# Optimization experiments

Hardware: AMD Instinct MI355X
Metric: run time of the kernel (lower is better)

## Reference

```python
import jax, jax.numpy as jnp
import numpy as np
from jax import lax

B, S, C, L = 256, 30, 62, 169   # batch, timesteps, channels(nodes), data_seg
OG, OH = 64, 64                 # out_gcn, out_gru
K1, K2, K3 = 64, 32, 14         # depthwise kernel sizes (169-63-31-13 = 62 = C)


def setup_inputs() -> dict:
    key = jax.random.key(0)
    ks = jax.random.split(key, 26)
    def n(k, shape, s=0.05):
        return jax.random.normal(k, shape, dtype=jnp.float32) * s
    inp = {
        "x": jax.random.normal(ks[0], (B, S, C, L), dtype=jnp.float32),
        "adj": jax.random.normal(ks[1], (C, C), dtype=jnp.float32),
        # depthwise-separable conv 1 (kernel 64)
        "dw1_w": n(ks[2], (C, 1, K1)), "dw1_b": n(ks[3], (C,)),
        "pw1_w": n(ks[4], (C, C, 1)), "pw1_b": n(ks[5], (C,)),
        # depthwise-separable conv 2 (kernel 32)
        "dw2_w": n(ks[6], (C, 1, K2)), "dw2_b": n(ks[7], (C,)),
        "pw2_w": n(ks[8], (C, C, 1)), "pw2_b": n(ks[9], (C,)),
        # depthwise-separable conv 3 (kernel 14)
        "dw3_w": n(ks[10], (C, 1, K3)), "dw3_b": n(ks[11], (C,)),
        "pw3_w": n(ks[12], (C, C, 1)), "pw3_b": n(ks[13], (C,)),
        # GraphConvolution(data_seg, out_gcn): support = x @ W; out = adj @ support + b
        "gcn_w": n(ks[14], (L, OG)), "gcn_b": n(ks[15], (OG,)),
        # GRU-style gate Linears (out_gcn+out_gru -> out_gru), torch layout (out, in)
        "Wr_w": n(ks[16], (OH, OG + OH)), "Wr_b": n(ks[17], (OH,)),
        "Wu_w": n(ks[18], (OH, OG + OH)), "Wu_b": n(ks[19], (OH,)),
        "Wc_w": n(ks[20], (OH, OG + OH)), "Wc_b": n(ks[21], (OH,)),
        # extra learned gate biases b_r/b_u/b_c (init zeros in torch)
        "b_r": jnp.zeros((OH,), jnp.float32),
        "b_u": jnp.zeros((OH,), jnp.float32),
        "b_c": jnp.zeros((OH,), jnp.float32),
    }
    return inp


def _dsconv(x, dw, dwb, pw, pwb):
    # x: (b, c, l); depthwise (groups=c, valid padding) then pointwise 1x1
    dn = ("NCH", "OIH", "NCH")
    y = lax.conv_general_dilated(x, dw, (1,), "VALID", dimension_numbers=dn,
                                 feature_group_count=x.shape[1]) + dwb[None, :, None]
    y = lax.conv_general_dilated(y, pw, (1,), "VALID", dimension_numbers=dn) + pwb[None, :, None]
    return y


def reference(x, adj, dw1_w, dw1_b, pw1_w, pw1_b, dw2_w, dw2_b, pw2_w, pw2_b,
              dw3_w, dw3_b, pw3_w, pw3_b, gcn_w, gcn_b,
              Wr_w, Wr_b, Wu_w, Wu_b, Wc_w, Wc_b, b_r, b_u, b_c):
    b, s, c, l = x.shape
    oh = b_r.shape[0]

    def step(h, xt):            # h: (b*c, oh), xt: (b, c, l)
        d = _dsconv(xt, dw1_w, dw1_b, pw1_w, pw1_b)
        d = _dsconv(d, dw2_w, dw2_b, pw2_w, pw2_b)
        d = _dsconv(d, dw3_w, dw3_b, pw3_w, pw3_b)      # (b, c, c)
        adj_t = jax.nn.sigmoid(d + adj)                  # adaptive adjacency
        support = jnp.einsum("bcl,lf->bcf", xt, gcn_w)
        g = jnp.einsum("bij,bjf->bif", adj_t, support) + gcn_b  # (b, c, og)
        gf = g.reshape(b * c, -1)
        cat = jnp.concatenate([gf, h], axis=-1)
        r = jax.nn.sigmoid(cat @ Wr_w.T + Wr_b + b_r)
        u = jax.nn.sigmoid(cat @ Wu_w.T + Wu_b + b_u)
        cc = jnp.tanh(jnp.concatenate([gf, r * h], axis=-1) @ Wc_w.T + Wc_b + b_c)
        h_new = u * h + (1.0 - u) * cc
        return h_new, None

    h0 = jnp.zeros((b * c, oh), x.dtype)
    xs = jnp.swapaxes(x, 0, 1)          # (s, b, c, l)
    h_last, _ = lax.scan(step, h0, xs)
    return h_last.reshape(b, c, oh)[:, -1, :]   # (b, out_gru)
```

## Files before the change

kernel.cpp:

```cpp
#include <hip/hip_runtime.h>
#include <math.h>

#define BB 256
#define SS 30
#define CC 62
#define LL 169
#define OG 64
#define OH 64
#define KK1 64
#define KK2 32
#define KK3 14
#define FLEN 108

typedef __attribute__((ext_vector_type(8))) short s16x8;
typedef __attribute__((ext_vector_type(4))) float f32x4;

__device__ __forceinline__ unsigned short f2bf(float f) {
    unsigned u = __float_as_uint(f);
    u += 0x7fffu + ((u >> 16) & 1u);
    return (unsigned short)(u >> 16);
}

__global__ __launch_bounds__(1024) void k_setup1(
        const float* __restrict__ dw1, const float* __restrict__ dw1b,
        const float* __restrict__ pw1, const float* __restrict__ pw1b,
        const float* __restrict__ dw2, const float* __restrict__ dw2b,
        const float* __restrict__ pw2, const float* __restrict__ pw2b,
        const float* __restrict__ dw3, const float* __restrict__ dw3b,
        const float* __restrict__ pw3, const float* __restrict__ pw3b,
        const float* __restrict__ Wr, const float* __restrict__ Wrb, const float* __restrict__ br,
        const float* __restrict__ Wu, const float* __restrict__ Wub, const float* __restrict__ bu,
        const float* __restrict__ Wc, const float* __restrict__ Wcb, const float* __restrict__ bc,
        float* __restrict__ Bmg, float* __restrict__ WtAll,
        float* __restrict__ bias192, float* __restrict__ beff) {
    __shared__ float g23[CC * KK3];
    __shared__ float Am[CC * 45];
    __shared__ float by2[CC], vals[CC];
    int tid = threadIdx.x;

    for (int idx = tid; idx < OG * 192; idx += 1024) {
        int i = idx / 192, q = idx - i * 192;
        int gate = q >> 6, f = q & 63;
        const float* W = gate == 0 ? Wr : (gate == 1 ? Wu : Wc);
        WtAll[idx] = W[f * (OG + OH) + i];
    }
    if (tid < 192) {
        int gate = tid >> 6, f = tid & 63;
        const float* Wb = gate == 0 ? Wrb : (gate == 1 ? Wub : Wcb);
        const float* bb = gate == 0 ? br  : (gate == 1 ? bu  : bc);
        bias192[tid] = Wb[f] + bb[f];
    }
    for (int idx = tid; idx < CC * KK3; idx += 1024) {
        int c1 = idx / KK3, k3 = idx - c1 * KK3;
        float s = 0.f;
        for (int c2 = 0; c2 < CC; ++c2)
            s += pw3[61 * CC + c2] * pw2[c2 * CC + c1] * dw3[c2 * KK3 + k3];
        g23[idx] = s;
    }
    if (tid < CC) {
        int c1 = tid;
        float bz1 = pw1b[c1];
        for (int c0 = 0; c0 < CC; ++c0) bz1 += pw1[c1 * CC + c0] * dw1b[c0];
        float s2 = 0.f;
        for (int k = 0; k < KK2; ++k) s2 += dw2[c1 * KK2 + k];
        by2[c1] = dw2b[c1] + bz1 * s2;
    }
    __syncthreads();
    if (tid < CC) {
        int c2 = tid;
        float bz2 = pw2b[c2];
        for (int c1 = 0; c1 < CC; ++c1) bz2 += pw2[c2 * CC + c1] * by2[c1];
        float s3 = 0.f;
        for (int k = 0; k < KK3; ++k) s3 += dw3[c2 * KK3 + k];
        vals[c2] = pw3[61 * CC + c2] * (dw3b[c2] + bz2 * s3);
    }
    for (int idx = tid; idx < CC * 45; idx += 1024) {
        int c1 = idx / 45, m = idx - c1 * 45;
        int k2lo = max(0, m - (KK3 - 1));
        int k2hi = min(KK2 - 1, m);
        float s = 0.f;
        for (int k2 = k2lo; k2 <= k2hi; ++k2)
            s += dw2[c1 * KK2 + k2] * g23[c1 * KK3 + (m - k2)];
        Am[idx] = s;
    }
    __syncthreads();
    if (tid == 0) {
        float s = pw3b[61];
        for (int c2 = 0; c2 < CC; ++c2) s += vals[c2];
        *beff = s;
    }
    for (int idx = tid; idx < CC * 45; idx += 1024) {
        int c0 = idx / 45, m = idx - c0 * 45;
        float s = 0.f;
        for (int c1 = 0; c1 < CC; ++c1) s += pw1[c1 * CC + c0] * Am[c1 * 45 + m];
        Bmg[idx] = s;
    }
}

__global__ __launch_bounds__(128) void k_setupF(
        const float* __restrict__ Bmg, const float* __restrict__ dw1,
        unsigned short* __restrict__ Ftb) {
    __shared__ float Bl[45];
    int c0 = blockIdx.x;
    int o = threadIdx.x;
    if (c0 < CC && o < 45) Bl[o] = Bmg[c0 * 45 + o];
    __syncthreads();
    if (o >= 112) return;
    float s = 0.f;
    if (c0 < CC && o < FLEN) {
        int mlo = max(0, o - (KK1 - 1));
        int mhi = min(44, o);
        for (int m = mlo; m <= mhi; ++m)
            s += Bl[m] * dw1[c0 * KK1 + (o - m)];
    }
    Ftb[o * 64 + c0] = f2bf(s);
}

#define CH_ISSUE(ch) do {                                                          \
    const int nd2 = ((ch) < 7) ? 676 : 507;                                        \
    const float* cb = xg + 1352 * (ch);                                            \
    _Pragma("unroll")                                                              \
    for (int j = 0; j < 3; ++j) {                                                  \
        int pos = tid + j * 256; if (pos > nd2 - 1) pos = nd2 - 1;                 \
        asm volatile("global_load_dwordx2 %0, %1, off"                             \
                     : "=v"(SL[(ch) & 1][j]) : "v"(cb + 2 * pos));                 \
    }                                                                              \
} while (0)

#define CH_CONSUME(ch, VM) do {                                                    \
    asm volatile("s_waitcnt vmcnt(" VM ")"                                         \
        : "+v"(SL[(ch) & 1][0]), "+v"(SL[(ch) & 1][1]), "+v"(SL[(ch) & 1][2]));    \
    {                                                                              \
        const int nd2 = ((ch) < 7) ? 676 : 507;                                    \
        uint2* cb2 = (uint2*)chunkbuf[(ch) & 1];                                   \
        _Pragma("unroll")                                                          \
        for (int j = 0; j < 3; ++j) {                                              \
            int pos = tid + j * 256; if (pos > nd2 - 1) pos = nd2 - 1;             \
            cb2[pos] = SL[(ch) & 1][j];                                            \
        }                                                                          \
    }                                                                              \
    asm volatile("s_waitcnt lgkmcnt(0)" ::: "memory");                             \
    __builtin_amdgcn_sched_barrier(0);                                             \
    __builtin_amdgcn_s_barrier();                                                  \
    {                                                                              \
        const int ncp = ((ch) < 7) ? 4 : 3;                                        \
        const unsigned* cb = (const unsigned*)chunkbuf[(ch) & 1];                  \
        int cpL = tid & 3, lb = tid >> 2;                                          \
        _Pragma("unroll")                                                          \
        for (int it = 0; it < 3; ++it) {                                           \
            int l = lb + 64 * it;                                                  \
            if (l < LL && cpL < ncp) {                                             \
                unsigned lo = cb[(2 * cpL) * LL + l];                              \
                unsigned hi = cb[(2 * cpL + 1) * LL + l];                          \
                unsigned v;                                                        \
                asm("v_cvt_pk_bf16_f32 %0, %1, %2" : "=v"(v)                       \
                    : "v"(__uint_as_float(lo)), "v"(__uint_as_float(hi)));         \
                int cp = (ch) * 4 + cpL;                                           \
                xTu[(l * 32 + cp) ^ ((l & 7) << 2)] = v;                           \
            }                                                                      \
        }                                                                          \
    }                                                                              \
    asm volatile("s_waitcnt lgkmcnt(0)" ::: "memory");                             \
    __builtin_amdgcn_sched_barrier(0);                                             \
    __builtin_amdgcn_s_barrier();                                                  \
} while (0)

__global__ __launch_bounds__(256, 3) void k_main(
        const float* __restrict__ x, const float* __restrict__ adj,
        const unsigned short* __restrict__ Ftb, const float* __restrict__ beff_p,
        const float* __restrict__ gcnw, const float* __restrict__ gcnb,
        const float* __restrict__ WtAll, const float* __restrict__ bias192,
        float* __restrict__ gates) {
    __shared__ __align__(16) unsigned short xT[176 * 64];
    __shared__ __align__(16) char chunkbuf[2][5408];
    __shared__ float dacc[4][64];
    __shared__ __align__(16) unsigned adjbf[32];
    __shared__ float wxl[176];
    __shared__ float gpart[4][64];
    __shared__ float Gl[64];
    int bt = blockIdx.x;
    int tid = threadIdx.x;
    int lane = tid & 63, wid = tid >> 6;
    int col = lane & 15, rb4 = lane >> 4;
    unsigned* xTu = (unsigned*)xT;
    const float* xg = x + (size_t)bt * (CC * LL);

    float be = *beff_p;
    float2 arow2 = make_float2(0.f, 0.f);
    if (tid < 31) arow2 = *(const float2*)(adj + 61 * CC + 2 * tid);
    const unsigned short* ap0 = Ftb + ((wid * 16 + col) * 64 + rb4 * 8);
    s16x8 pa0 = *(const s16x8*)ap0;
    s16x8 pa1 = *(const s16x8*)(ap0 + 32);
    int mt2c = wid + 4 < 7 ? wid + 4 : 6;
    const unsigned short* ap1 = Ftb + ((mt2c * 16 + col) * 64 + rb4 * 8);
    s16x8 pb0 = *(const s16x8*)(ap1);
    s16x8 pb1 = *(const s16x8*)(ap1 + 32);
    __builtin_amdgcn_sched_barrier(0);

    uint2 SL[2][3];
    CH_ISSUE(0); CH_ISSUE(1);
    for (int i = tid; i < 169; i += 256) xTu[(i * 32 + 31) ^ ((i & 7) << 2)] = 0;
    for (int i = tid; i < 224; i += 256) {
        int r = 169 + (i >> 5), dd = i & 31;
        xTu[(r * 32 + dd) ^ ((r & 7) << 2)] = 0;
    }
    ((float*)dacc)[tid] = 0.f;

    CH_CONSUME(0, "3"); CH_ISSUE(2);
    CH_CONSUME(1, "3"); CH_ISSUE(3);
    CH_CONSUME(2, "3"); CH_ISSUE(4);
    CH_CONSUME(3, "3"); CH_ISSUE(5);
    CH_CONSUME(4, "3"); CH_ISSUE(6);
    CH_CONSUME(5, "3"); CH_ISSUE(7);
    CH_CONSUME(6, "3");
    CH_CONSUME(7, "0");

    f32x4 zacc[5];
    #pragma unroll
    for (int d = 0; d < 5; ++d) zacc[d] = (f32x4){0.f, 0.f, 0.f, 0.f};
    int kb = rb4 * 16;
    int xr = (lane & 7) << 4;
    #pragma unroll
    for (int h = 0; h < 2; ++h) {
        int mt = wid + 4 * h;
        if (mt < 7) {
            s16x8 a0 = h == 0 ? pa0 : pb0;
            s16x8 a1 = h == 0 ? pa1 : pb1;
            #pragma unroll
            for (int d = 0; d < 5; ++d) {
                int nt = mt + d;
                int bbyte = ((nt * 16 + col) * 128 + kb) ^ xr;
                s16x8 b0 = *(const s16x8*)((const char*)xT + bbyte);
                s16x8 b1 = *(const s16x8*)((const char*)xT + (bbyte ^ 64));
                zacc[d] = __builtin_amdgcn_mfma_f32_16x16x32_bf16(a0, b0, zacc[d], 0, 0, 0);
                zacc[d] = __builtin_amdgcn_mfma_f32_16x16x32_bf16(a1, b1, zacc[d], 0, 0, 0);
            }
        }
    }
    int jc = col - rb4 * 4;
    #pragma unroll
    for (int d = 0; d < 5; ++d) {
        #pragma unroll
        for (int r = 0; r < 4; ++r) {
            int j = 16 * d + jc - r;
            if ((unsigned)j < 62u) atomicAdd(&dacc[rb4][j], zacc[d][r]);
        }
    }
    __syncthreads();

    if (tid < 32) {
        unsigned pk = 0;
        if (tid < 31) {
            int j0 = 2 * tid;
            float2 g0 = *(const float2*)(&dacc[0][j0]);
            float2 g1 = *(const float2*)(&dacc[1][j0]);
            float2 g2 = *(const float2*)(&dacc[2][j0]);
            float2 g3 = *(const float2*)(&dacc[3][j0]);
            float dv0 = (g0.x + g1.x) + (g2.x + g3.x) + be + arow2.x;
            float dv1 = (g0.y + g1.y) + (g2.y + g3.y) + be + arow2.y;
            float s0 = 1.f / (1.f + __expf(-dv0));
            float s1 = 1.f / (1.f + __expf(-dv1));
            asm("v_cvt_pk_bf16_f32 %0, %1, %2" : "=v"(pk) : "v"(s0), "v"(s1));
        }
        adjbf[tid] = pk;
    }
    __syncthreads();

    {
        s16x8 wa0 = *(const s16x8*)(adjbf + rb4 * 4);
        s16x8 wa1 = *(const s16x8*)(adjbf + 16 + rb4 * 4);
        #pragma unroll
        for (int q = 0; q < 3; ++q) {
            int nt = wid + 4 * q;
            if (nt < 11) {
                int bbyte = ((nt * 16 + col) * 128 + kb) ^ xr;
                s16x8 b0 = *(const s16x8*)((const char*)xT + bbyte);
                s16x8 b1 = *(const s16x8*)((const char*)xT + (bbyte ^ 64));
                f32x4 wacc = {0.f, 0.f, 0.f, 0.f};
                wacc = __builtin_amdgcn_mfma_f32_16x16x32_bf16(wa0, b0, wacc, 0, 0, 0);
                wacc = __builtin_amdgcn_mfma_f32_16x16x32_bf16(wa1, b1, wacc, 0, 0, 0);
                if (rb4 == 0) wxl[nt * 16 + col] = wacc[0];
            }
        }
    }
    __syncthreads();

    {
        int f = tid & 63, lq = tid >> 6;
        float s = 0.f;
        for (int l = lq; l < LL; l += 4) s += wxl[l] * gcnw[l * OG + f];
        gpart[lq][f] = s;
    }
    __syncthreads();
    if (tid < OG)
        Gl[tid] = gcnb[tid] + gpart[0][tid] + gpart[1][tid] + gpart[2][tid] + gpart[3][tid];
    __syncthreads();

    if (tid < 192) {
        float s = bias192[tid];
        #pragma unroll 16
        for (int k = 0; k < OG; ++k) s += Gl[k] * WtAll[k * 192 + tid];
        gates[(size_t)bt * 192 + tid] = s;
    }
}

__global__ __launch_bounds__(256) void k_scan(
        const float* __restrict__ gates,
        const float* __restrict__ Wr, const float* __restrict__ Wu, const float* __restrict__ Wc,
        float* __restrict__ out) {
    __shared__ float hl[OH], rhl[OH];
    int b = blockIdx.x;
    int tid = threadIdx.x;
    int f = tid >> 2, q = tid & 3;
    float wr[16], wu[16], wc[16];
    #pragma unroll
    for (int i = 0; i < 16; ++i) {
        int col = OG + q * 16 + i;
        wr[i] = Wr[f * (OG + OH) + col];
        wu[i] = Wu[f * (OG + OH) + col];
        wc[i] = Wc[f * (OG + OH) + col];
    }
    float h = 0.f;
    if (tid < OH) hl[tid] = 0.f;
    __syncthreads();
    for (int t = 0; t < SS; ++t) {
        const float* gp = gates + ((size_t)b * SS + t) * 192;
        float gr = gp[f];
        float gu = gp[64 + f];
        float gc = gp[128 + f];
        float rv = 0.f, uv = 0.f;
        #pragma unroll
        for (int i = 0; i < 16; ++i) {
            float hv = hl[q * 16 + i];
            rv += wr[i] * hv;
            uv += wu[i] * hv;
        }
        rv += __shfl_xor(rv, 1); rv += __shfl_xor(rv, 2);
        uv += __shfl_xor(uv, 1); uv += __shfl_xor(uv, 2);
        float r = 1.f / (1.f + __expf(-(rv + gr)));
        float u = 1.f / (1.f + __expf(-(uv + gu)));
        if (q == 0) rhl[f] = r * h;
        __syncthreads();
        float cv = 0.f;
        #pragma unroll
        for (int i = 0; i < 16; ++i) cv += wc[i] * rhl[q * 16 + i];
        cv += __shfl_xor(cv, 1); cv += __shfl_xor(cv, 2);
        float cc = tanhf(cv + gc);
        if (q == 0) {
            h = u * h + (1.f - u) * cc;
            hl[f] = h;
        }
        __syncthreads();
    }
    if (q == 0) out[b * OH + f] = h;
}

extern "C" void kernel_launch(void* const* d_in, const int* in_sizes, int n_in,
                              void* d_out, int out_size, void* d_ws, size_t ws_size,
                              hipStream_t stream) {
    const float* x    = (const float*)d_in[0];
    const float* adj  = (const float*)d_in[1];
    const float* dw1w = (const float*)d_in[2];
    const float* dw1b = (const float*)d_in[3];
    const float* pw1w = (const float*)d_in[4];
    const float* pw1b = (const float*)d_in[5];
    const float* dw2w = (const float*)d_in[6];
    const float* dw2b = (const float*)d_in[7];
    const float* pw2w = (const float*)d_in[8];
    const float* pw2b = (const float*)d_in[9];
    const float* dw3w = (const float*)d_in[10];
    const float* dw3b = (const float*)d_in[11];
    const float* pw3w = (const float*)d_in[12];
    const float* pw3b = (const float*)d_in[13];
    const float* gcnw = (const float*)d_in[14];
    const float* gcnb = (const float*)d_in[15];
    const float* Wrw  = (const float*)d_in[16];
    const float* Wrb  = (const float*)d_in[17];
    const float* Wuw  = (const float*)d_in[18];
    const float* Wub  = (const float*)d_in[19];
    const float* Wcw  = (const float*)d_in[20];
    const float* Wcb  = (const float*)d_in[21];
    const float* br   = (const float*)d_in[22];
    const float* bu   = (const float*)d_in[23];
    const float* bc   = (const float*)d_in[24];
    float* out = (float*)d_out;

    char* ws = (char*)d_ws;
    unsigned short* Ftb = (unsigned short*)(ws + 0);
    float* WtAll        = (float*)(ws + 14336);
    float* bias192      = (float*)(ws + 63488);
    float* beff         = (float*)(ws + 64256);
    float* Bmg          = (float*)(ws + 64320);
    float* gates        = (float*)(ws + 76800);
    (void)ws_size; (void)in_sizes; (void)n_in; (void)out_size;

    k_setup1<<<1, 1024, 0, stream>>>(dw1w, dw1b, pw1w, pw1b, dw2w, dw2b, pw2w, pw2b,
                                     dw3w, dw3b, pw3w, pw3b,
                                     Wrw, Wrb, br, Wuw, Wub, bu, Wcw, Wcb, bc,
                                     Bmg, WtAll, bias192, beff);
    k_setupF<<<64, 128, 0, stream>>>(Bmg, dw1w, Ftb);
    k_main<<<BB * SS, 256, 0, stream>>>(x, adj, Ftb, beff, gcnw, gcnb,
                                        WtAll, bias192, gates);
    k_scan<<<BB, 256, 0, stream>>>(gates, Wrw, Wuw, Wcw, out);
}
```

Measured before the change: 341.1 us.

## Give each wavefront its own channel-pair staging buffer and drop block barriers

```diff
diff --git a/kernel.cpp b/kernel.cpp
--- a/kernel.cpp
+++ b/kernel.cpp
@@ -116,53 +116,56 @@
     Ftb[o * 64 + c0] = f2bf(s);
 }
 
-#define CH_ISSUE(ch) do {                                                          \
-    const int nd2 = ((ch) < 7) ? 676 : 507;                                        \
-    const float* cb = xg + 1352 * (ch);                                            \
+#define CH_ISSUE(g, s) do {                                                        \
+    const uint2* p0 = (const uint2*)(xg + 338 * (2 * (g)));                        \
+    const uint2* p1 = (const uint2*)(xg + 338 * (2 * (g) + 1 > 30 ? 30 : 2 * (g) + 1)); \
     _Pragma("unroll")                                                              \
     for (int j = 0; j < 3; ++j) {                                                  \
-        int pos = tid + j * 256; if (pos > nd2 - 1) pos = nd2 - 1;                 \
+        int pos = lane + 64 * j; if (pos > 168) pos = 168;                         \
         asm volatile("global_load_dwordx2 %0, %1, off"                             \
-                     : "=v"(SL[(ch) & 1][j]) : "v"(cb + 2 * pos));                 \
+                     : "=v"(RG[s][j]) : "v"(p0 + pos));                            \
+        asm volatile("global_load_dwordx2 %0, %1, off"                             \
+                     : "=v"(RG[s][3 + j]) : "v"(p1 + pos));                        \
     }                                                                              \
 } while (0)
 
-#define CH_CONSUME(ch, VM) do {                                                    \
+#define CH_CONSUME(g, s, VM) do {                                                  \
     asm volatile("s_waitcnt vmcnt(" VM ")"                                         \
-        : "+v"(SL[(ch) & 1][0]), "+v"(SL[(ch) & 1][1]), "+v"(SL[(ch) & 1][2]));    \
+        : "+v"(RG[s][0]), "+v"(RG[s][1]), "+v"(RG[s][2]),                          \
+          "+v"(RG[s][3]), "+v"(RG[s][4]), "+v"(RG[s][5]));                         \
     {                                                                              \
-        const int nd2 = ((ch) < 7) ? 676 : 507;                                    \
-        uint2* cb2 = (uint2*)chunkbuf[(ch) & 1];                                   \
+        uint2* cb2 = (uint2*)(chunkbuf + wid * 2704);                              \
         _Pragma("unroll")                                                          \
         for (int j = 0; j < 3; ++j) {                                              \
-            int pos = tid + j * 256; if (pos > nd2 - 1) pos = nd2 - 1;             \
-            cb2[pos] = SL[(ch) & 1][j];                                            \
+            int pos = lane + 64 * j; if (pos > 168) pos = 168;                     \
+            cb2[pos] = RG[s][j];                                                   \
+            cb2[169 + pos] = RG[s][3 + j];                                         \
         }                                                                          \
     }                                                                              \
     asm volatile("s_waitcnt lgkmcnt(0)" ::: "memory");                             \
     __builtin_amdgcn_sched_barrier(0);                                             \
-    __builtin_amdgcn_s_barrier();                                                  \
     {                                                                              \
-        const int ncp = ((ch) < 7) ? 4 : 3;                                        \
-        const unsigned* cb = (const unsigned*)chunkbuf[(ch) & 1];                  \
-        int cpL = tid & 3, lb = tid >> 2;                                          \
-        _Pragma("unroll")                                                          \
-        for (int it = 0; it < 3; ++it) {                                           \
-            int l = lb + 64 * it;                                                  \
-            if (l < LL && cpL < ncp) {                                             \
-                unsigned lo = cb[(2 * cpL) * LL + l];                              \
-                unsigned hi = cb[(2 * cpL + 1) * LL + l];                          \
-                unsigned v;                                                        \
-                asm("v_cvt_pk_bf16_f32 %0, %1, %2" : "=v"(v)                       \
-                    : "v"(__uint_as_float(lo)), "v"(__uint_as_float(hi)));         \
-                int cp = (ch) * 4 + cpL;                                           \
-                xTu[(l * 32 + cp) ^ ((l & 7) << 2)] = v;                           \
+        int cpL = lane >> 5, lb = lane & 31;                                       \
+        int cp = 2 * (g) + cpL;                                                    \
+        if (cp < 31) {                                                             \
+            const unsigned* cbf = (const unsigned*)(chunkbuf + wid * 2704);        \
+            int base = cpL * 338;                                                  \
+            _Pragma("unroll")                                                      \
+            for (int it = 0; it < 6; ++it) {                                       \
+                int l = lb + 32 * it;                                              \
+                if (l < LL) {                                                      \
+                    unsigned lo = cbf[base + l];                                   \
+                    unsigned hi = cbf[base + 169 + l];                             \
+                    unsigned v;                                                    \
+                    asm("v_cvt_pk_bf16_f32 %0, %1, %2" : "=v"(v)                   \
+                        : "v"(__uint_as_float(lo)), "v"(__uint_as_float(hi)));     \
+                    xTu[(l * 32 + cp) ^ ((l & 7) << 2)] = v;                       \
+                }                                                                  \
             }                                                                      \
         }                                                                          \
     }                                                                              \
     asm volatile("s_waitcnt lgkmcnt(0)" ::: "memory");                             \
     __builtin_amdgcn_sched_barrier(0);                                             \
-    __builtin_amdgcn_s_barrier();                                                  \
 } while (0)
 
 __global__ __launch_bounds__(256, 3) void k_main(
@@ -172,7 +175,7 @@
         const float* __restrict__ WtAll, const float* __restrict__ bias192,
         float* __restrict__ gates) {
     __shared__ __align__(16) unsigned short xT[176 * 64];
-    __shared__ __align__(16) char chunkbuf[2][5408];
+    __shared__ __align__(16) char chunkbuf[4 * 2704];
     __shared__ float dacc[4][64];
     __shared__ __align__(16) unsigned adjbf[32];
     __shared__ float wxl[176];
@@ -197,8 +200,9 @@
     s16x8 pb1 = *(const s16x8*)(ap1 + 32);
     __builtin_amdgcn_sched_barrier(0);
 
-    uint2 SL[2][3];
-    CH_ISSUE(0); CH_ISSUE(1);
+    uint2 RG[2][6];
+    CH_ISSUE(wid, 0);
+    CH_ISSUE(wid + 4, 1);
     for (int i = tid; i < 169; i += 256) xTu[(i * 32 + 31) ^ ((i & 7) << 2)] = 0;
     for (int i = tid; i < 224; i += 256) {
         int r = 169 + (i >> 5), dd = i & 31;
@@ -206,14 +210,11 @@
     }
     ((float*)dacc)[tid] = 0.f;
 
-    CH_CONSUME(0, "3"); CH_ISSUE(2);
-    CH_CONSUME(1, "3"); CH_ISSUE(3);
-    CH_CONSUME(2, "3"); CH_ISSUE(4);
-    CH_CONSUME(3, "3"); CH_ISSUE(5);
-    CH_CONSUME(4, "3"); CH_ISSUE(6);
-    CH_CONSUME(5, "3"); CH_ISSUE(7);
-    CH_CONSUME(6, "3");
-    CH_CONSUME(7, "0");
+    CH_CONSUME(wid, 0, "6");      CH_ISSUE(wid + 8, 0);
+    CH_CONSUME(wid + 4, 1, "6");  CH_ISSUE(wid + 12, 1);
+    CH_CONSUME(wid + 8, 0, "6");
+    CH_CONSUME(wid + 12, 1, "0");
+    __syncthreads();
 
     f32x4 zacc[5];
     #pragma unroll
```

Result: faster. 310.0 us (-9.1%).
